# Performance work log

Measured on AMD Instinct MI355X. Metric: run time of the kernel, lower is better.

## Reference

```python
import jax, jax.numpy as jnp
import numpy as np

NV, NE, NI, D = 100000, 20000, 600000, 128

def setup_inputs() -> dict:
    key = jax.random.key(0)
    ks = jax.random.split(key, 16)
    inp = {
        'vfeat': jax.random.normal(ks[0], (NV, D), jnp.float32),
        'efeat': jax.random.normal(ks[1], (NE, D), jnp.float32),
        # positive regularization weights/sums (HNHN degree-based normalizers)
        'v_reg_weight': jax.random.uniform(ks[2], (NV, 1), jnp.float32, 0.5, 1.5),
        'v_reg_sum': jax.random.uniform(ks[3], (NV, 1), jnp.float32, 0.5, 1.5),
        'e_reg_weight': jax.random.uniform(ks[4], (NE, 1), jnp.float32, 0.5, 1.5),
        'e_reg_sum': jax.random.uniform(ks[5], (NE, 1), jnp.float32, 0.5, 1.5),
        'node_idx': jax.random.randint(ks[6], (NI,), 0, NV),
        'hedge_idx': jax.random.randint(ks[7], (NI,), 0, NE),
    }
    s = 1.0 / np.sqrt(D)
    inp['W1'] = jax.random.uniform(ks[8], (D, D), jnp.float32, -s, s)
    inp['b1'] = jax.random.uniform(ks[9], (D,), jnp.float32, -s, s)
    inp['Wve'] = jax.random.uniform(ks[10], (D, D), jnp.float32, -s, s)
    inp['bve'] = jax.random.uniform(ks[11], (D,), jnp.float32, -s, s)
    inp['Wev'] = jax.random.uniform(ks[12], (D, D), jnp.float32, -s, s)
    inp['bev'] = jax.random.uniform(ks[13], (D,), jnp.float32, -s, s)
    return inp


def reference(vfeat, efeat, v_reg_weight, v_reg_sum, e_reg_weight, e_reg_sum,
              node_idx, hedge_idx, W1, b1, Wve, bve, Wev, bev):
    # vertex projection (vtx_lin_1layer)
    feat_v = vfeat @ W1.T + b1                      # [NV, Dv]
    # node -> hyperedge pass ('in' etype)
    Wh_n = feat_v @ Wve.T + bve                     # [NV, De]
    w_in = v_reg_weight[node_idx] / e_reg_sum[hedge_idx]   # [NI, 1]
    feat_e = jax.ops.segment_sum(w_in * Wh_n[node_idx], hedge_idx,
                                 num_segments=NE)   # [NE, De]
    # hyperedge -> node pass ('con' etype)
    Wh_e = feat_e @ Wev.T + bev                     # [NE, Dv]
    w_con = e_reg_weight[hedge_idx] / v_reg_sum[node_idx]  # [NI, 1]
    feat_v_out = jax.ops.segment_sum(w_con * Wh_e[hedge_idx], node_idx,
                                     num_segments=NV)  # [NV, Dv]
    return feat_v_out
```

## Files before the change

kernel.cpp:

```cpp
#include <hip/hip_runtime.h>

#define D 128
#define PADE 16
#define PADV 4

typedef unsigned short ushort_t;
typedef short short8 __attribute__((ext_vector_type(8)));
typedef ushort_t ushort8v __attribute__((ext_vector_type(8)));
typedef float f32x4 __attribute__((ext_vector_type(4)));

static __device__ __forceinline__ unsigned short f2bf(float f){
  unsigned int b = __float_as_uint(f);
  unsigned int r = (b + 0x7FFFu + ((b >> 16) & 1u)) >> 16;
  return (unsigned short)r;
}
static __device__ __forceinline__ float bf2f(unsigned short u){
  return __uint_as_float(((unsigned int)u) << 16);
}


__global__ void k_u1(const float* __restrict__ W1, const float* __restrict__ Wve,
                     const float* __restrict__ b1, const float* __restrict__ bve,
                     float* __restrict__ Wcf, float* __restrict__ bc,
                     const float* __restrict__ vfeat, ushort_t* __restrict__ vbf, int nvd,
                     const int* __restrict__ node_idx, const int* __restrict__ hedge_idx, int ni,
                     int* __restrict__ cnt_e_pad, int* __restrict__ cnt_v_pad,
                     int* __restrict__ rank_e, int* __restrict__ rank_v,
                     int vb, int cb){
  int t = threadIdx.x;
  int i = blockIdx.x;
  if (i < 128){
    int r = i;
    if (t < D){
      float acc = 0.f;
      for (int k = 0; k < D; ++k) acc += Wve[r * D + k] * W1[k * D + t];
      Wcf[r * D + t] = acc;
      if (t == 0){
        float s = 0.f;
        for (int k = 0; k < D; ++k) s += Wve[r * D + k] * b1[k];
        bc[r] = s + bve[r];
      }
    }
    return;
  }
  int j = i - 128;
  int total = vb + cb;
  long a0 = (long)j * vb / total, a1 = (long)(j + 1) * vb / total;
  if (a1 != a0){
    size_t base = (size_t)a0 * 8192;
#pragma unroll
    for (int c = 0; c < 4; ++c){
      size_t e8 = base + (size_t)c * 2048 + (size_t)t * 8;
      if (e8 < (size_t)nvd){
        float4 v0 = *(const float4*)&vfeat[e8];
        float4 v1 = *(const float4*)&vfeat[e8 + 4];
        ushort8v h;
        h[0] = f2bf(v0.x); h[1] = f2bf(v0.y); h[2] = f2bf(v0.z); h[3] = f2bf(v0.w);
        h[4] = f2bf(v1.x); h[5] = f2bf(v1.y); h[6] = f2bf(v1.z); h[7] = f2bf(v1.w);
        *(ushort8v*)&vbf[e8] = h;
      }
    }
  } else {
    int idx = (int)(j - a0) * 256 + t;
    if (idx < ni){
      int n = node_idx[idx], h = hedge_idx[idx];
      rank_e[idx] = atomicAdd(&cnt_e_pad[h * PADE], 1);
      rank_v[idx] = atomicAdd(&cnt_v_pad[n * PADV], 1);
    }
  }
}


__device__ __forceinline__ void scan_partial_body(const int* cnt, int n, int stride,
                                                  int* bsum, int b){
  __shared__ int s[256];
  int t = threadIdx.x;
  int base = b * 1024;
  int acc = 0;
  for (int j = t; j < 1024; j += 256){
    int idx = base + j;
    if (idx < n) acc += cnt[(size_t)idx * stride];
  }
  s[t] = acc; __syncthreads();
  for (int o = 128; o > 0; o >>= 1){
    if (t < o) s[t] += s[t + o];
    __syncthreads();
  }
  if (t == 0) bsum[b] = s[0];
}

__global__ void k_scan_partial2(const int* __restrict__ ce, int ne, int* __restrict__ bse,
                                const int* __restrict__ cv, int nv, int* __restrict__ bsv,
                                int nbe){
  if ((int)blockIdx.x < nbe) scan_partial_body(ce, ne, PADE, bse, blockIdx.x);
  else                       scan_partial_body(cv, nv, PADV, bsv, blockIdx.x - nbe);
}

__device__ __forceinline__ void scan_bsums_body(int* bsum, int nb){
  __shared__ int s[256];
  int t = threadIdx.x;
  int runbase = 0;
  for (int base = 0; base < nb; base += 256){
    int v = (base + t < nb) ? bsum[base + t] : 0;
    s[t] = v;
    __syncthreads();
    for (int o = 1; o < 256; o <<= 1){
      int x = (t >= o) ? s[t - o] : 0;
      __syncthreads();
      s[t] += x;
      __syncthreads();
    }
    int total = s[255];
    if (base + t < nb) bsum[base + t] = runbase + (s[t] - v);
    __syncthreads();
    runbase += total;
  }
}

__global__ void k_scan_bsums2(int* __restrict__ bse, int nbe, int* __restrict__ bsv, int nbv){
  if (blockIdx.x == 0) scan_bsums_body(bse, nbe);
  else                 scan_bsums_body(bsv, nbv);
}

__device__ __forceinline__ void scan_final_body(const int* cnt, int n, int stride,
                                                const int* bsum, int* off, int* cout, int b){
  __shared__ int s[256];
  int t = threadIdx.x;
  int base = b * 1024 + t * 4;
  int v0 = (base + 0 < n) ? cnt[(size_t)(base + 0) * stride] : 0;
  int v1 = (base + 1 < n) ? cnt[(size_t)(base + 1) * stride] : 0;
  int v2 = (base + 2 < n) ? cnt[(size_t)(base + 2) * stride] : 0;
  int v3 = (base + 3 < n) ? cnt[(size_t)(base + 3) * stride] : 0;
  int lsum = v0 + v1 + v2 + v3;
  s[t] = lsum; __syncthreads();
  for (int o = 1; o < 256; o <<= 1){
    int x = (t >= o) ? s[t - o] : 0;
    __syncthreads();
    s[t] += x;
    __syncthreads();
  }
  int excl = s[t] - lsum + bsum[b];
  if (base + 0 < n){ off[base + 0] = excl;                cout[base + 0] = v0; }
  if (base + 1 < n){ off[base + 1] = excl + v0;           cout[base + 1] = v1; }
  if (base + 2 < n){ off[base + 2] = excl + v0 + v1;      cout[base + 2] = v2; }
  if (base + 3 < n){ off[base + 3] = excl + v0 + v1 + v2; cout[base + 3] = v3; }
}

__global__ void k_scan_final2(const int* __restrict__ ce, int ne, const int* __restrict__ bse,
                              int* __restrict__ off_e, int* __restrict__ cnt_e,
                              const int* __restrict__ cv, int nv, const int* __restrict__ bsv,
                              int* __restrict__ off_v, int* __restrict__ cnt_v, int nbe){
  if ((int)blockIdx.x < nbe) scan_final_body(ce, ne, PADE, bse, off_e, cnt_e, blockIdx.x);
  else                       scan_final_body(cv, nv, PADV, bsv, off_v, cnt_v, blockIdx.x - nbe);
}


__global__ void k_u2(const float* __restrict__ Wev, const float* __restrict__ Wcf,
                     const float* __restrict__ bc,
                     ushort_t* __restrict__ Wcc, float* __restrict__ bvec1,
                     const int* __restrict__ node_idx, const int* __restrict__ hedge_idx,
                     const int* __restrict__ rank_e, int ni,
                     const int* __restrict__ off_e, int* __restrict__ elist_v){
  int t = threadIdx.x;
  int i = blockIdx.x;
  if (i < 128){
    int r = i;
    if (t < D){
      float acc = 0.f;
      for (int k = 0; k < D; ++k) acc += Wev[r * D + k] * Wcf[k * D + t];
      Wcc[r * D + t] = f2bf(acc);
      if (t == 0){
        float s = 0.f;
        for (int k = 0; k < D; ++k) s += Wev[r * D + k] * bc[k];
        bvec1[r] = s;
      }
    }
  } else {
    int idx = (i - 128) * 256 + t;
    if (idx < ni){
      int pe = off_e[hedge_idx[idx]] + rank_e[idx];
      __builtin_nontemporal_store(node_idx[idx], &elist_v[pe]);
    }
  }
}


__global__ void k_u3(const ushort_t* __restrict__ vbf,
                     const int* __restrict__ off_e, const int* __restrict__ cnt_e,
                     const int* __restrict__ elist,
                     const float* __restrict__ vrw, const float* __restrict__ ers,
                     float* __restrict__ agg, float* __restrict__ wsum,
                     int ne, int sb, int total,
                     const int* __restrict__ node_idx, const int* __restrict__ hedge_idx,
                     const int* __restrict__ rank_v, int ni,
                     const int* __restrict__ off_v, int* __restrict__ vlist_e){
  int i = blockIdx.x;
  long a0 = (long)i * sb / total, a1 = (long)(i + 1) * sb / total;
  if (a1 != a0){
    int tid = threadIdx.x;
    int seg = (int)a0 * 16 + (tid >> 4);
    if (seg >= ne) return;
    int l16 = tid & 15;
    int s = off_e[seg], n = cnt_e[seg];
    float inv = 1.0f / ers[seg];

    float acc[8];
#pragma unroll
    for (int c = 0; c < 8; ++c) acc[c] = 0.f;
    float wa = 0.f;

    int j = 0;
    for (; j + 2 <= n; j += 2){
      int r0 = elist[s + j];
      int r1 = elist[s + j + 1];
      float w0 = vrw[r0];
      float w1 = vrw[r1];
      ushort8v x0 = *(const ushort8v*)&vbf[(size_t)r0 * D + l16 * 8];
      ushort8v x1 = *(const ushort8v*)&vbf[(size_t)r1 * D + l16 * 8];
      wa += w0 + w1;
#pragma unroll
      for (int c = 0; c < 8; ++c) acc[c] += w0 * bf2f(x0[c]) + w1 * bf2f(x1[c]);
    }
    if (j < n){
      int r0 = elist[s + j];
      float w0 = vrw[r0];
      ushort8v x0 = *(const ushort8v*)&vbf[(size_t)r0 * D + l16 * 8];
      wa += w0;
#pragma unroll
      for (int c = 0; c < 8; ++c) acc[c] += w0 * bf2f(x0[c]);
    }

    float* dp = &agg[(size_t)seg * D + l16 * 8];
    float4 o0, o1;
    o0.x = acc[0] * inv; o0.y = acc[1] * inv; o0.z = acc[2] * inv; o0.w = acc[3] * inv;
    o1.x = acc[4] * inv; o1.y = acc[5] * inv; o1.z = acc[6] * inv; o1.w = acc[7] * inv;
    *(float4*)dp = o0;
    *(float4*)(dp + 4) = o1;
    if (l16 == 0) wsum[seg] = wa * inv;
  } else {
    int idx = (int)(i - a0) * 256 + threadIdx.x;
    if (idx < ni){
      int pv = off_v[node_idx[idx]] + rank_v[idx];
      __builtin_nontemporal_store(hedge_idx[idx], &vlist_e[pv]);
    }
  }
}


__global__ __launch_bounds__(256, 2)
void k_gemm_rs(const float* __restrict__ A, const ushort_t* __restrict__ Wb,
               const float* __restrict__ wsum, const float* __restrict__ bvec1,
               const float* __restrict__ bev, ushort_t* __restrict__ out, int M){
  __shared__ ushort_t Al[64 * D];

  const int t = threadIdx.x;
  const int w = t >> 6;
  const int l = t & 63;
  const int l15 = l & 15;
  const int lh = l >> 4;

  short8 breg[4][8];
#pragma unroll
  for (int kc = 0; kc < 4; ++kc)
#pragma unroll
    for (int n0 = 0; n0 < 8; ++n0)
      breg[kc][n0] = *(const short8*)&Wb[(n0 * 16 + l15) * D + kc * 32 + lh * 8];

  float bv1_r[8], bev_r[8];
#pragma unroll
  for (int n0 = 0; n0 < 8; ++n0){
    bv1_r[n0] = bvec1[n0 * 16 + l15];
    bev_r[n0] = bev[n0 * 16 + l15];
  }

  const int r_st = t >> 2;
  const int q_st = t & 3;
  const int ntile = (M + 63) >> 6;

  for (int tile = blockIdx.x; tile < ntile; tile += gridDim.x){
    const int row0 = tile << 6;
    __syncthreads();
    {
      int r = row0 + r_st;
      ushort8v h[4];
      if (r < M){
        const float4* src = (const float4*)&A[(size_t)r * D + q_st * 32];
        float4 v[8];
#pragma unroll
        for (int ii = 0; ii < 8; ++ii) v[ii] = src[ii];
#pragma unroll
        for (int c = 0; c < 4; ++c){
          h[c][0] = f2bf(v[2*c].x);   h[c][1] = f2bf(v[2*c].y);
          h[c][2] = f2bf(v[2*c].z);   h[c][3] = f2bf(v[2*c].w);
          h[c][4] = f2bf(v[2*c+1].x); h[c][5] = f2bf(v[2*c+1].y);
          h[c][6] = f2bf(v[2*c+1].z); h[c][7] = f2bf(v[2*c+1].w);
        }
      } else {
#pragma unroll
        for (int c = 0; c < 4; ++c) h[c] = (ushort8v){0,0,0,0,0,0,0,0};
      }
#pragma unroll
      for (int c = 0; c < 4; ++c){
        int col = q_st * 32 + c * 8;
        int swz = col ^ ((r_st & 7) << 3);
        *(ushort8v*)&Al[r_st * D + swz] = h[c];
      }
    }
    __syncthreads();

    f32x4 acc[8];
#pragma unroll
    for (int n0 = 0; n0 < 8; ++n0) acc[n0] = (f32x4){0.f, 0.f, 0.f, 0.f};

#pragma unroll
    for (int kc = 0; kc < 4; ++kc){
      const int arow = w * 16 + l15;
      const int acol = (kc * 32 + lh * 8) ^ ((l15 & 7) << 3);
      short8 a = *(const short8*)&Al[arow * D + acol];
#pragma unroll
      for (int n0 = 0; n0 < 8; ++n0)
        acc[n0] = __builtin_amdgcn_mfma_f32_16x16x32_bf16(a, breg[kc][n0], acc[n0], 0, 0, 0);
    }

    const int rbase = row0 + w * 16 + lh * 4;
    float w4[4];
#pragma unroll
    for (int rg = 0; rg < 4; ++rg)
      w4[rg] = (rbase + rg < M) ? wsum[rbase + rg] : 0.f;
#pragma unroll
    for (int n0 = 0; n0 < 8; ++n0){
      const int colo = n0 * 16 + l15;
#pragma unroll
      for (int rg = 0; rg < 4; ++rg){
        int row = rbase + rg;
        if (row < M)
          out[(size_t)row * D + colo] = f2bf(acc[n0][rg] + w4[rg] * bv1_r[n0] + bev_r[n0]);
      }
    }
  }
}


__global__ void k_scatter2(const ushort_t* __restrict__ src,
                           const int* __restrict__ off, const int* __restrict__ cnt,
                           const int* __restrict__ list,
                           const float* __restrict__ wnum, const float* __restrict__ dsum,
                           float* __restrict__ dst, int nseg){
  int tid = threadIdx.x;
  int seg = blockIdx.x * 16 + (tid >> 4);
  if (seg >= nseg) return;
  int l16 = tid & 15;
  int s = off[seg], n = cnt[seg];
  float inv = 1.0f / dsum[seg];

  float acc[8];
#pragma unroll
  for (int c = 0; c < 8; ++c) acc[c] = 0.f;

  int j = 0;
  for (; j + 2 <= n; j += 2){
    int r0 = list[s + j];
    int r1 = list[s + j + 1];
    float w0 = wnum[r0] * inv;
    float w1 = wnum[r1] * inv;
    ushort8v x0 = *(const ushort8v*)&src[(size_t)r0 * D + l16 * 8];
    ushort8v x1 = *(const ushort8v*)&src[(size_t)r1 * D + l16 * 8];
#pragma unroll
    for (int c = 0; c < 8; ++c) acc[c] += w0 * bf2f(x0[c]) + w1 * bf2f(x1[c]);
  }
  if (j < n){
    int r0 = list[s + j];
    float w0 = wnum[r0] * inv;
    ushort8v x0 = *(const ushort8v*)&src[(size_t)r0 * D + l16 * 8];
#pragma unroll
    for (int c = 0; c < 8; ++c) acc[c] += w0 * bf2f(x0[c]);
  }

  float* dp = &dst[(size_t)seg * D + l16 * 8];
  float4 o0, o1;
  o0.x = acc[0]; o0.y = acc[1]; o0.z = acc[2]; o0.w = acc[3];
  o1.x = acc[4]; o1.y = acc[5]; o1.z = acc[6]; o1.w = acc[7];
  *(float4*)dp = o0;
  *(float4*)(dp + 4) = o1;
}


static inline int cdiv(int a, int b){ return (a + b - 1) / b; }

extern "C" void kernel_launch(void* const* d_in, const int* in_sizes, int n_in,
                              void* d_out, int out_size, void* d_ws, size_t ws_size,
                              hipStream_t stream){
  const float* vfeat        = (const float*)d_in[0];
  const float* v_reg_weight = (const float*)d_in[2];
  const float* v_reg_sum    = (const float*)d_in[3];
  const float* e_reg_weight = (const float*)d_in[4];
  const float* e_reg_sum    = (const float*)d_in[5];
  const int*   node_idx     = (const int*)d_in[6];
  const int*   hedge_idx    = (const int*)d_in[7];
  const float* W1  = (const float*)d_in[8];
  const float* b1  = (const float*)d_in[9];
  const float* Wve = (const float*)d_in[10];
  const float* bve = (const float*)d_in[11];
  const float* Wev = (const float*)d_in[12];
  const float* bev = (const float*)d_in[13];

  const int NV = in_sizes[2];
  const int NE = in_sizes[4];
  const int NI = in_sizes[6];
  const int NVD = NV * D;

  char* p = (char*)d_ws;
  auto alloc = [&](size_t nbytes) -> void* {
    void* q = (void*)p;
    p += (nbytes + 255) & ~(size_t)255;
    return q;
  };

  char* zstart = p;
  int* cnt_e_pad = (int*)alloc((size_t)NE * PADE * 4);
  int* cnt_v_pad = (int*)alloc((size_t)NV * PADV * 4);
  size_t zbytes = (size_t)(p - zstart);

  int* cnt_e  = (int*)alloc((size_t)NE * 4);
  int* cnt_v  = (int*)alloc((size_t)NV * 4);
  int* off_e  = (int*)alloc((size_t)NE * 4);
  int* off_v  = (int*)alloc((size_t)NV * 4);
  int* bsum_e = (int*)alloc(1024 * 4);
  int* bsum_v = (int*)alloc(1024 * 4);
  int* rank_e = (int*)alloc((size_t)NI * 4);
  int* rank_v = (int*)alloc((size_t)NI * 4);
  int* elist_v = (int*)alloc((size_t)NI * 4);
  int* vlist_e = (int*)alloc((size_t)NI * 4);
  float* Wcf     = (float*)alloc((size_t)D * D * 4);
  float* bc      = (float*)alloc((size_t)D * 4);
  ushort_t* Wcc  = (ushort_t*)alloc((size_t)D * D * 2);
  float* bvec1   = (float*)alloc((size_t)D * 4);
  ushort_t* Wh_e = (ushort_t*)alloc((size_t)NE * D * 2);

  ushort_t* vbf  = (ushort_t*)d_out;
  float*    agg  = (float*)((char*)d_out + (size_t)NVD * 2);
  float*    wsum = (float*)((char*)d_out + (size_t)NVD * 2 + (size_t)NE * D * 4);

  hipMemsetAsync(zstart, 0, zbytes, stream);

  int cb = cdiv(NI, 256);
  int vb = cdiv(NVD, 8192);
  k_u1<<<128 + vb + cb, 256, 0, stream>>>(W1, Wve, b1, bve, Wcf, bc,
                                          vfeat, vbf, NVD,
                                          node_idx, hedge_idx, NI,
                                          cnt_e_pad, cnt_v_pad, rank_e, rank_v,
                                          vb, cb);

  int nbe = cdiv(NE, 1024), nbv = cdiv(NV, 1024);
  k_scan_partial2<<<nbe + nbv, 256, 0, stream>>>(cnt_e_pad, NE, bsum_e,
                                                 cnt_v_pad, NV, bsum_v, nbe);
  k_scan_bsums2<<<2, 256, 0, stream>>>(bsum_e, nbe, bsum_v, nbv);
  k_scan_final2<<<nbe + nbv, 256, 0, stream>>>(cnt_e_pad, NE, bsum_e, off_e, cnt_e,
                                               cnt_v_pad, NV, bsum_v, off_v, cnt_v, nbe);

  k_u2<<<128 + cb, 256, 0, stream>>>(Wev, Wcf, bc, Wcc, bvec1,
                                     node_idx, hedge_idx, rank_e, NI,
                                     off_e, elist_v);

  int sb = cdiv(NE, 16);
  int u3_total = sb + cb;
  k_u3<<<u3_total, 256, 0, stream>>>(vbf, off_e, cnt_e, elist_v,
                                     v_reg_weight, e_reg_sum,
                                     agg, wsum, NE, sb, u3_total,
                                     node_idx, hedge_idx, rank_v, NI,
                                     off_v, vlist_e);

  k_gemm_rs<<<cdiv(NE, 64), 256, 0, stream>>>(agg, Wcc, wsum, bvec1, bev, Wh_e, NE);

  k_scatter2<<<cdiv(NV, 16), 256, 0, stream>>>(Wh_e, off_v, cnt_v, vlist_e,
                                               e_reg_weight, v_reg_sum,
                                               (float*)d_out, NV);
}
```

Baseline: 179.7 us.

## Privatize hyperedge counting into shared-memory histograms with packed 16-bit counters

Hyperedge incidence counting and rank assignment move from per-element global atomics on a padded counter array to 16 dedicated blocks. Each block builds a shared-memory histogram with two 16-bit counters packed per word, then publishes its block base with 64-bit global atomics and adds it to the local ranks. This cuts global atomic contention and removes the padded count array and the count copy in the scan. The trade-off is that the 16 blocks each process a large serial chunk and may lengthen the critical path of the first kernel.

Measured after the change: 239.7 us. 1.33x slower.

```diff
diff --git a/kernel.cpp b/kernel.cpp
--- a/kernel.cpp
+++ b/kernel.cpp
@@ -1,8 +1,9 @@
 #include <hip/hip_runtime.h>
 
 #define D 128
-#define PADE 16
 #define PADV 4
+#define EB 16
+#define EHW 10240
 
 typedef unsigned short ushort_t;
 typedef short short8 __attribute__((ext_vector_type(8)));
@@ -19,16 +20,52 @@
 }
 
 
-__global__ void k_u1(const float* __restrict__ W1, const float* __restrict__ Wve,
-                     const float* __restrict__ b1, const float* __restrict__ bve,
-                     float* __restrict__ Wcf, float* __restrict__ bc,
-                     const float* __restrict__ vfeat, ushort_t* __restrict__ vbf, int nvd,
-                     const int* __restrict__ node_idx, const int* __restrict__ hedge_idx, int ni,
-                     int* __restrict__ cnt_e_pad, int* __restrict__ cnt_v_pad,
-                     int* __restrict__ rank_e, int* __restrict__ rank_v,
-                     int vb, int cb){
+__global__ __launch_bounds__(256)
+void k_u1(const float* __restrict__ W1, const float* __restrict__ Wve,
+          const float* __restrict__ b1, const float* __restrict__ bve,
+          float* __restrict__ Wcf, float* __restrict__ bc,
+          const float* __restrict__ vfeat, ushort_t* __restrict__ vbf, int nvd,
+          const int* __restrict__ node_idx, const int* __restrict__ hedge_idx,
+          int ni, int ne,
+          int* __restrict__ cnt_e, unsigned* __restrict__ bbase,
+          int* __restrict__ cnt_v_pad,
+          int* __restrict__ rank_e, int* __restrict__ rank_v,
+          int eprv, int vb, int cb){
+  __shared__ unsigned hist[EHW];
   int t = threadIdx.x;
   int i = blockIdx.x;
+
+  if (i < EB){
+    if (eprv){
+      int per = (ni + EB - 1) / EB;
+      int i0 = i * per;
+      int i1 = i0 + per; if (i1 > ni) i1 = ni;
+      for (int k = t; k < EHW; k += 256) hist[k] = 0;
+      __syncthreads();
+      for (int j = i0 + t; j < i1; j += 256){
+        int e = hedge_idx[j];
+        unsigned old = atomicAdd(&hist[e >> 1], (e & 1) ? 0x10000u : 1u);
+        rank_e[j] = (e & 1) ? (int)(old >> 16) : (int)(old & 0xFFFFu);
+      }
+      __syncthreads();
+      int nw = (ne + 1) >> 1;
+      unsigned* bb = bbase + (size_t)i * (EHW * 2);
+      for (int k = t; k < nw; k += 256){
+        unsigned w = hist[k];
+        if (w){
+          unsigned long long add = ((unsigned long long)(w >> 16) << 32) | (w & 0xFFFFu);
+          unsigned long long old = atomicAdd((unsigned long long*)(cnt_e + 2 * k), add);
+          bb[2 * k]     = (unsigned)old;
+          bb[2 * k + 1] = (unsigned)(old >> 32);
+        }
+      }
+      __syncthreads();
+      for (int j = i0 + t; j < i1; j += 256)
+        rank_e[j] += (int)bb[hedge_idx[j]];
+    }
+    return;
+  }
+  i -= EB;
   if (i < 128){
     int r = i;
     if (t < D){
@@ -43,9 +80,9 @@
     }
     return;
   }
-  int j = i - 128;
+  i -= 128;
   int total = vb + cb;
-  long a0 = (long)j * vb / total, a1 = (long)(j + 1) * vb / total;
+  long a0 = (long)i * vb / total, a1 = (long)(i + 1) * vb / total;
   if (a1 != a0){
     size_t base = (size_t)a0 * 8192;
 #pragma unroll
@@ -61,11 +98,14 @@
       }
     }
   } else {
-    int idx = (int)(j - a0) * 256 + t;
+    int idx = (int)(i - a0) * 256 + t;
     if (idx < ni){
-      int n = node_idx[idx], h = hedge_idx[idx];
-      rank_e[idx] = atomicAdd(&cnt_e_pad[h * PADE], 1);
+      int n = node_idx[idx];
       rank_v[idx] = atomicAdd(&cnt_v_pad[n * PADV], 1);
+      if (!eprv){
+        int h = hedge_idx[idx];
+        rank_e[idx] = atomicAdd(&cnt_e[h], 1);
+      }
     }
   }
 }
@@ -92,7 +132,7 @@
 __global__ void k_scan_partial2(const int* __restrict__ ce, int ne, int* __restrict__ bse,
                                 const int* __restrict__ cv, int nv, int* __restrict__ bsv,
                                 int nbe){
-  if ((int)blockIdx.x < nbe) scan_partial_body(ce, ne, PADE, bse, blockIdx.x);
+  if ((int)blockIdx.x < nbe) scan_partial_body(ce, ne, 1, bse, blockIdx.x);
   else                       scan_partial_body(cv, nv, PADV, bsv, blockIdx.x - nbe);
 }
 
@@ -140,17 +180,17 @@
     __syncthreads();
   }
   int excl = s[t] - lsum + bsum[b];
-  if (base + 0 < n){ off[base + 0] = excl;                cout[base + 0] = v0; }
-  if (base + 1 < n){ off[base + 1] = excl + v0;           cout[base + 1] = v1; }
-  if (base + 2 < n){ off[base + 2] = excl + v0 + v1;      cout[base + 2] = v2; }
-  if (base + 3 < n){ off[base + 3] = excl + v0 + v1 + v2; cout[base + 3] = v3; }
+  if (base + 0 < n){ off[base + 0] = excl;                if (cout) cout[base + 0] = v0; }
+  if (base + 1 < n){ off[base + 1] = excl + v0;           if (cout) cout[base + 1] = v1; }
+  if (base + 2 < n){ off[base + 2] = excl + v0 + v1;      if (cout) cout[base + 2] = v2; }
+  if (base + 3 < n){ off[base + 3] = excl + v0 + v1 + v2; if (cout) cout[base + 3] = v3; }
 }
 
 __global__ void k_scan_final2(const int* __restrict__ ce, int ne, const int* __restrict__ bse,
-                              int* __restrict__ off_e, int* __restrict__ cnt_e,
+                              int* __restrict__ off_e,
                               const int* __restrict__ cv, int nv, const int* __restrict__ bsv,
                               int* __restrict__ off_v, int* __restrict__ cnt_v, int nbe){
-  if ((int)blockIdx.x < nbe) scan_final_body(ce, ne, PADE, bse, off_e, cnt_e, blockIdx.x);
+  if ((int)blockIdx.x < nbe) scan_final_body(ce, ne, 1, bse, off_e, (int*)nullptr, blockIdx.x);
   else                       scan_final_body(cv, nv, PADV, bsv, off_v, cnt_v, blockIdx.x - nbe);
 }
 
@@ -417,11 +457,11 @@
   };
 
   char* zstart = p;
-  int* cnt_e_pad = (int*)alloc((size_t)NE * PADE * 4);
+  int* cnt_e     = (int*)alloc(((size_t)NE + 2) * 4);
   int* cnt_v_pad = (int*)alloc((size_t)NV * PADV * 4);
   size_t zbytes = (size_t)(p - zstart);
 
-  int* cnt_e  = (int*)alloc((size_t)NE * 4);
+  unsigned* bbase = (unsigned*)alloc((size_t)EB * EHW * 2 * 4);
   int* cnt_v  = (int*)alloc((size_t)NV * 4);
   int* off_e  = (int*)alloc((size_t)NE * 4);
   int* off_v  = (int*)alloc((size_t)NV * 4);
@@ -445,17 +485,19 @@
 
   int cb = cdiv(NI, 256);
   int vb = cdiv(NVD, 8192);
-  k_u1<<<128 + vb + cb, 256, 0, stream>>>(W1, Wve, b1, bve, Wcf, bc,
-                                          vfeat, vbf, NVD,
-                                          node_idx, hedge_idx, NI,
-                                          cnt_e_pad, cnt_v_pad, rank_e, rank_v,
-                                          vb, cb);
+  int eprv = (NE <= 2 * EHW) ? 1 : 0;
+  k_u1<<<EB + 128 + vb + cb, 256, 0, stream>>>(W1, Wve, b1, bve, Wcf, bc,
+                                               vfeat, vbf, NVD,
+                                               node_idx, hedge_idx, NI, NE,
+                                               cnt_e, bbase, cnt_v_pad,
+                                               rank_e, rank_v,
+                                               eprv, vb, cb);
 
   int nbe = cdiv(NE, 1024), nbv = cdiv(NV, 1024);
-  k_scan_partial2<<<nbe + nbv, 256, 0, stream>>>(cnt_e_pad, NE, bsum_e,
+  k_scan_partial2<<<nbe + nbv, 256, 0, stream>>>(cnt_e, NE, bsum_e,
                                                  cnt_v_pad, NV, bsum_v, nbe);
   k_scan_bsums2<<<2, 256, 0, stream>>>(bsum_e, nbe, bsum_v, nbv);
-  k_scan_final2<<<nbe + nbv, 256, 0, stream>>>(cnt_e_pad, NE, bsum_e, off_e, cnt_e,
+  k_scan_final2<<<nbe + nbv, 256, 0, stream>>>(cnt_e, NE, bsum_e, off_e,
                                                cnt_v_pad, NV, bsum_v, off_v, cnt_v, nbe);
 
   k_u2<<<128 + cb, 256, 0, stream>>>(Wev, Wcf, bc, Wcc, bvec1,
```
